# Performance work log

Measured on AMD Instinct MI355X. Metric: run time of the kernel, lower is better.

## Reference

```python
import jax, jax.numpy as jnp
import numpy as np
import math

B, T, P, E, H = 4, 64, 256, 512, 8
D = E // H
LN_EPS = 1e-5


def setup_inputs() -> dict:
    key = jax.random.key(0)
    ks = jax.random.split(key, 6)
    s = 0.02  # weight init scale
    return {
        "x": jax.random.normal(ks[0], (B, T, P, E), jnp.float32),
        "Wq": jax.random.normal(ks[1], (E, E), jnp.float32) * s,
        "bq": jnp.zeros((E,), jnp.float32),
        "Wk": jax.random.normal(ks[2], (E, E), jnp.float32) * s,
        "bk": jnp.zeros((E,), jnp.float32),
        "Wv": jax.random.normal(ks[3], (E, E), jnp.float32) * s,
        "bv": jnp.zeros((E,), jnp.float32),
        "Wo": jax.random.normal(ks[4], (E, E), jnp.float32) * s,
        "bo": jnp.zeros((E,), jnp.float32),
        "ln_g": jnp.ones((E,), jnp.float32),
        "ln_b": jnp.zeros((E,), jnp.float32),
    }


def _proj(x, W, b):
    # torch nn.Linear: y = x @ W.T + b
    return jnp.einsum('btpe,fe->btpf', x, W) + b


def _heads(y):
    # b t p (h d) -> b p h t d
    b, t, p, e = y.shape
    return y.reshape(b, t, p, H, D).transpose(0, 2, 3, 1, 4)


def reference(x, Wq, bq, Wk, bk, Wv, bv, Wo, bo, ln_g, ln_b):
    b, t, p, e = x.shape
    q = _heads(_proj(x, Wq, bq))  # [B,P,H,T,D]
    k = _heads(_proj(x, Wk, bk))
    v = _heads(_proj(x, Wv, bv))

    scores = jnp.einsum('bphtd,bphsd->bphts', q, k) / math.sqrt(D)
    causal_mask = jnp.triu(jnp.ones((t, t), dtype=bool), k=1)  # True above diag
    scores = jnp.where(causal_mask, -jnp.inf, scores)
    attn = jax.nn.softmax(scores, axis=-1)
    o = jnp.einsum('bphts,bphsd->bphtd', attn, v)

    # b p h t d -> b t p (h d)
    o = o.transpose(0, 3, 1, 2, 4).reshape(b, t, p, e)
    attn_out = jnp.einsum('btpe,fe->btpf', o, Wo) + bo

    y = x + attn_out
    # AdaptiveNormalizer with conditioning=None -> plain LayerNorm over E
    mu = jnp.mean(y, axis=-1, keepdims=True)
    var = jnp.var(y, axis=-1, keepdims=True)
    return (y - mu) * jax.lax.rsqrt(var + LN_EPS) * ln_g + ln_b
```

## Files before the change

### kernel.cpp

```cpp
#include <hip/hip_runtime.h>
#include <stdint.h>

#define B_ 4
#define T_ 64
#define P_ 256
#define E_ 512
#define H_ 8
#define D_ 64
#define NF 1536
#define MCH 16384

typedef unsigned short u16;
typedef __attribute__((ext_vector_type(8))) __bf16 bf16x8;
typedef __attribute__((ext_vector_type(4))) float f32x4;

__device__ __forceinline__ u16 f2bf(float x) {
  union { float f; uint32_t u; } a; a.f = x;
  uint32_t u = a.u;
  uint32_t r = (u + 0x7FFFu + ((u >> 16) & 1u)) >> 16;
  return (u16)r;
}

__device__ __forceinline__ bf16x8 ld8(const u16* p) {
  union { uint4 u; bf16x8 b; } t;
  t.u = *reinterpret_cast<const uint4*>(p);
  return t.b;
}

typedef __attribute__((address_space(3))) void lds_void;
typedef __attribute__((address_space(1))) void g_void;
__device__ __forceinline__ void gl_lds16(const void* g, void* l) {
  __builtin_amdgcn_global_load_lds((g_void*)g, (lds_void*)l, 16, 0, 0);
}

__device__ __forceinline__ f32x4 mfma16(bf16x8 a, bf16x8 b, f32x4 c) {
  return __builtin_amdgcn_mfma_f32_16x16x32_bf16(a, b, c, 0, 0, 0);
}

__global__ void cvt_bf16(const float* __restrict__ src, u16* __restrict__ dst, int n8) {
  int i = blockIdx.x * blockDim.x + threadIdx.x;
  if (i >= n8) return;
  const float4* s = reinterpret_cast<const float4*>(src) + (size_t)i * 2;
  float4 a = s[0], b = s[1];
  union { u16 u[8]; uint4 v; } t;
  t.u[0] = f2bf(a.x); t.u[1] = f2bf(a.y); t.u[2] = f2bf(a.z); t.u[3] = f2bf(a.w);
  t.u[4] = f2bf(b.x); t.u[5] = f2bf(b.y); t.u[6] = f2bf(b.z); t.u[7] = f2bf(b.w);
  reinterpret_cast<uint4*>(dst)[i] = t.v;
}

__global__ void cvt_w(const float* __restrict__ Wq, const float* __restrict__ Wk,
                      const float* __restrict__ Wv, const float* __restrict__ Wo,
                      u16* __restrict__ wqkv, u16* __restrict__ wobf) {
  int idx = blockIdx.x * blockDim.x + threadIdx.x;
  int w = idx >> 15;
  int off = idx & 32767;
  const float* s = (w == 0) ? Wq : (w == 1) ? Wk : (w == 2) ? Wv : Wo;
  const float4* sp = reinterpret_cast<const float4*>(s) + (size_t)off * 2;
  float4 a = sp[0], b = sp[1];
  union { u16 u[8]; uint4 v; } t;
  t.u[0] = f2bf(a.x); t.u[1] = f2bf(a.y); t.u[2] = f2bf(a.z); t.u[3] = f2bf(a.w);
  t.u[4] = f2bf(b.x); t.u[5] = f2bf(b.y); t.u[6] = f2bf(b.z); t.u[7] = f2bf(b.w);
  if (w < 3) reinterpret_cast<uint4*>(wqkv)[w * 32768 + off] = t.v;
  else       reinterpret_cast<uint4*>(wobf)[off] = t.v;
}

__global__ __launch_bounds__(256) void k1_qkv(
    const u16* __restrict__ xbf,
    const u16* __restrict__ wqkv,
    const float* __restrict__ bq, const float* __restrict__ bk, const float* __restrict__ bv,
    u16* __restrict__ qkv)
{
  __shared__ u16 As[2][128 * 64];
  __shared__ u16 Bs[2][128 * 64];
  const int tid = threadIdx.x;
  const int lane = tid & 63;
  const int wid = tid >> 6;
  const int m0 = blockIdx.y * 128;
  const int n0 = blockIdx.x * 128;
  const int wm = (wid >> 1) * 64;
  const int wn = (wid & 1) * 64;
  const int g4 = lane >> 4, l15 = lane & 15;
  const int lrow = lane >> 3;
  const int lcol = (lane & 7) * 8;

  f32x4 acc[4][4];
#pragma unroll
  for (int i = 0; i < 4; i++)
#pragma unroll
    for (int j = 0; j < 4; j++) { f32x4 z = {0.f, 0.f, 0.f, 0.f}; acc[i][j] = z; }

  const u16* ga = xbf + (size_t)m0 * E_;
  const u16* gb = wqkv + (size_t)n0 * E_;

  auto stage = [&](int buf, int kt) {
    const int k0 = kt * 64;
#pragma unroll
    for (int p = 0; p < 4; ++p) {
      const int ch = wid * 4 + p;
      const int r = ch * 8 + lrow;
      gl_lds16(ga + (size_t)r * E_ + k0 + lcol, &As[buf][ch * 512]);
      gl_lds16(gb + (size_t)r * E_ + k0 + lcol, &Bs[buf][ch * 512]);
    }
  };

  stage(0, 0);
  __syncthreads();
  int cur = 0;
  for (int kt = 0; kt < 8; ++kt) {
    if (kt < 7) stage(cur ^ 1, kt + 1);
#pragma unroll
    for (int ks = 0; ks < 2; ++ks) {
      const int fc = ks * 32 + g4 * 8;
      bf16x8 af[4], bfr[4];
#pragma unroll
      for (int mi = 0; mi < 4; mi++) af[mi] = ld8(&As[cur][(wm + mi * 16 + l15) * 64 + fc]);
#pragma unroll
      for (int ni = 0; ni < 4; ni++) bfr[ni] = ld8(&Bs[cur][(wn + ni * 16 + l15) * 64 + fc]);
#pragma unroll
      for (int mi = 0; mi < 4; mi++)
#pragma unroll
        for (int ni = 0; ni < 4; ni++)
          acc[mi][ni] = mfma16(af[mi], bfr[ni], acc[mi][ni]);
    }
    __syncthreads();
    cur ^= 1;
  }
#pragma unroll
  for (int ni = 0; ni < 4; ni++) {
    const int fcol = n0 + wn + ni * 16 + l15;
    const float bias = fcol < 512 ? bq[fcol] : (fcol < 1024 ? bk[fcol - 512] : bv[fcol - 1024]);
#pragma unroll
    for (int mi = 0; mi < 4; mi++)
#pragma unroll
      for (int r = 0; r < 4; r++) {
        const int row = m0 + wm + mi * 16 + g4 * 4 + r;
        qkv[(size_t)row * NF + fcol] = f2bf(acc[mi][ni][r] + bias);
      }
  }
}

__global__ __launch_bounds__(256) void k2_attn(
    const u16* __restrict__ qkv,
    u16* __restrict__ o)
{
  __shared__ u16 Pl[4][64 * 72];
  const int tid = threadIdx.x, lane = tid & 63, wid = tid >> 6;
  const int gw = blockIdx.x * 4 + wid;
  const int b = gw >> 11;
  const int g = gw & 2047;
  const int h = g & 7, p = g >> 3;
  const int g4 = lane >> 4;
  const size_t ts = (size_t)P_ * NF;
  const u16* qb = qkv + (size_t)b * MCH * NF + (size_t)p * NF + h * D_;
  const u16* kb = qb + 512;
  const u16* vb = qb + 1024;
  u16* ob = o + (size_t)b * MCH * E_;

  bf16x8 qf[4][2], kf[4][2];
#pragma unroll
  for (int i = 0; i < 4; i++)
#pragma unroll
    for (int ks = 0; ks < 2; ks++) {
      const int rr = i * 16 + (lane & 15);
      const int dc = ks * 32 + g4 * 8;
      qf[i][ks] = ld8(qb + (size_t)rr * ts + dc);
      kf[i][ks] = ld8(kb + (size_t)rr * ts + dc);
    }
  f32x4 S[4][4];
#pragma unroll
  for (int i = 0; i < 4; i++)
#pragma unroll
    for (int j = 0; j < 4; j++) { f32x4 z = {0.f, 0.f, 0.f, 0.f}; S[i][j] = z; }
#pragma unroll
  for (int ks = 0; ks < 2; ks++)
#pragma unroll
    for (int mi = 0; mi < 4; mi++)
#pragma unroll
      for (int ni = 0; ni < 4; ni++)
        S[mi][ni] = mfma16(qf[mi][ks], kf[ni][ks], S[mi][ni]);

  u16* pw = &Pl[wid][0];
#pragma unroll
  for (int mi = 0; mi < 4; mi++)
#pragma unroll
    for (int r = 0; r < 4; r++) {
      const int t = mi * 16 + g4 * 4 + r;
      float v[4]; float mx = -1e30f;
#pragma unroll
      for (int ni = 0; ni < 4; ni++) {
        const int s = ni * 16 + (lane & 15);
        v[ni] = (s <= t) ? S[mi][ni][r] * 0.125f : -1e30f;
        mx = fmaxf(mx, v[ni]);
      }
      mx = fmaxf(mx, __shfl_xor(mx, 1));
      mx = fmaxf(mx, __shfl_xor(mx, 2));
      mx = fmaxf(mx, __shfl_xor(mx, 4));
      mx = fmaxf(mx, __shfl_xor(mx, 8));
      float sum = 0.f; float pv[4];
#pragma unroll
      for (int ni = 0; ni < 4; ni++) {
        const int s = ni * 16 + (lane & 15);
        pv[ni] = (s <= t) ? __expf(v[ni] - mx) : 0.f;
        sum += pv[ni];
      }
      sum += __shfl_xor(sum, 1);
      sum += __shfl_xor(sum, 2);
      sum += __shfl_xor(sum, 4);
      sum += __shfl_xor(sum, 8);
      const float inv = 1.0f / sum;
#pragma unroll
      for (int ni = 0; ni < 4; ni++) {
        const int s = ni * 16 + (lane & 15);
        pw[t * 72 + s] = f2bf(pv[ni] * inv);
      }
    }
  __syncthreads();

  f32x4 O[4][4];
#pragma unroll
  for (int i = 0; i < 4; i++)
#pragma unroll
    for (int j = 0; j < 4; j++) { f32x4 z = {0.f, 0.f, 0.f, 0.f}; O[i][j] = z; }
#pragma unroll
  for (int ks = 0; ks < 2; ks++) {
    bf16x8 pa[4], vf[4];
#pragma unroll
    for (int mi = 0; mi < 4; mi++)
      pa[mi] = ld8(pw + (mi * 16 + (lane & 15)) * 72 + ks * 32 + g4 * 8);
#pragma unroll
    for (int ni = 0; ni < 4; ni++) {
      union { u16 u[8]; bf16x8 b; } tv;
#pragma unroll
      for (int j = 0; j < 8; j++) {
        const int s = ks * 32 + g4 * 8 + j;
        tv.u[j] = vb[(size_t)s * ts + ni * 16 + (lane & 15)];
      }
      vf[ni] = tv.b;
    }
#pragma unroll
    for (int mi = 0; mi < 4; mi++)
#pragma unroll
      for (int ni = 0; ni < 4; ni++)
        O[mi][ni] = mfma16(pa[mi], vf[ni], O[mi][ni]);
  }
#pragma unroll
  for (int mi = 0; mi < 4; mi++)
#pragma unroll
    for (int ni = 0; ni < 4; ni++)
#pragma unroll
      for (int r = 0; r < 4; r++) {
        const int t = mi * 16 + g4 * 4 + r;
        const int d = ni * 16 + (lane & 15);
        ob[((size_t)t * P_ + p) * E_ + h * D_ + d] = f2bf(O[mi][ni][r]);
      }
}

__global__ __launch_bounds__(512) void k3_out(
    const u16* __restrict__ obf,
    const u16* __restrict__ wo,
    const float* __restrict__ bo,
    const float* __restrict__ x,
    const float* __restrict__ lng, const float* __restrict__ lnb,
    float* __restrict__ out)
{
  __shared__ u16 As[2][128 * 32];
  __shared__ u16 Bs[2][512 * 32];
  __shared__ float redS[128][8];
  __shared__ float redQ[128][8];
  const int tid = threadIdx.x, lane = tid & 63, wid = tid >> 6;
  const int m0 = blockIdx.x * 128;
  const int g4 = lane >> 4, l15 = lane & 15;
  const int lr = lane >> 2;
  const int lc = (lane & 3) * 8;

  f32x4 acc[8][4];
#pragma unroll
  for (int i = 0; i < 8; i++)
#pragma unroll
    for (int j = 0; j < 4; j++) { f32x4 z = {0.f, 0.f, 0.f, 0.f}; acc[i][j] = z; }

  const u16* ga = obf + (size_t)m0 * E_;

  auto stage = [&](int buf, int kt) {
    const int k0 = kt * 32;
    gl_lds16(ga + (size_t)(wid * 16 + lr) * E_ + k0 + lc, &As[buf][wid * 512]);
#pragma unroll
    for (int p = 0; p < 4; ++p) {
      const int ch = wid * 4 + p;
      gl_lds16(wo + (size_t)(ch * 16 + lr) * E_ + k0 + lc, &Bs[buf][ch * 512]);
    }
  };

  stage(0, 0);
  __syncthreads();
  int cur = 0;
  for (int kt = 0; kt < 16; ++kt) {
    if (kt < 15) stage(cur ^ 1, kt + 1);
    const int fc = g4 * 8;
    bf16x8 af[8], bfr[4];
#pragma unroll
    for (int mi = 0; mi < 8; mi++) af[mi] = ld8(&As[cur][(mi * 16 + l15) * 32 + fc]);
#pragma unroll
    for (int ni = 0; ni < 4; ni++) bfr[ni] = ld8(&Bs[cur][(wid * 64 + ni * 16 + l15) * 32 + fc]);
#pragma unroll
    for (int mi = 0; mi < 8; mi++)
#pragma unroll
      for (int ni = 0; ni < 4; ni++)
        acc[mi][ni] = mfma16(af[mi], bfr[ni], acc[mi][ni]);
    __syncthreads();
    cur ^= 1;
  }

  float gg[4], bb[4], bof[4];
#pragma unroll
  for (int ni = 0; ni < 4; ni++) {
    const int f = wid * 64 + ni * 16 + l15;
    gg[ni] = lng[f]; bb[ni] = lnb[f]; bof[ni] = bo[f];
  }
#pragma unroll
  for (int mi = 0; mi < 8; mi++)
#pragma unroll
    for (int r = 0; r < 4; r++) {
      const int n = m0 + mi * 16 + g4 * 4 + r;
#pragma unroll
      for (int ni = 0; ni < 4; ni++) {
        const int f = wid * 64 + ni * 16 + l15;
        acc[mi][ni][r] += bof[ni] + x[(size_t)n * E_ + f];
      }
    }
#pragma unroll
  for (int mi = 0; mi < 8; mi++)
#pragma unroll
    for (int r = 0; r < 4; r++) {
      float s = 0.f, q = 0.f;
#pragma unroll
      for (int ni = 0; ni < 4; ni++) { const float y = acc[mi][ni][r]; s += y; q += y * y; }
      s += __shfl_xor(s, 1); q += __shfl_xor(q, 1);
      s += __shfl_xor(s, 2); q += __shfl_xor(q, 2);
      s += __shfl_xor(s, 4); q += __shfl_xor(q, 4);
      s += __shfl_xor(s, 8); q += __shfl_xor(q, 8);
      if (l15 == 0) {
        const int rl = mi * 16 + g4 * 4 + r;
        redS[rl][wid] = s; redQ[rl][wid] = q;
      }
    }
  __syncthreads();
#pragma unroll
  for (int mi = 0; mi < 8; mi++)
#pragma unroll
    for (int r = 0; r < 4; r++) {
      const int rl = mi * 16 + g4 * 4 + r;
      float Sx = 0.f, Qx = 0.f;
#pragma unroll
      for (int w = 0; w < 8; w++) { Sx += redS[rl][w]; Qx += redQ[rl][w]; }
      const float mean = Sx * (1.0f / 512.0f);
      const float var = Qx * (1.0f / 512.0f) - mean * mean;
      const float rs = rsqrtf(var + 1e-5f);
      const int n = m0 + rl;
#pragma unroll
      for (int ni = 0; ni < 4; ni++) {
        const int f = wid * 64 + ni * 16 + l15;
        out[(size_t)n * E_ + f] = (acc[mi][ni][r] - mean) * rs * gg[ni] + bb[ni];
      }
    }
}

extern "C" void kernel_launch(void* const* d_in, const int* in_sizes, int n_in,
                              void* d_out, int out_size, void* d_ws, size_t ws_size,
                              hipStream_t stream) {
  const float* x   = (const float*)d_in[0];
  const float* Wq  = (const float*)d_in[1];
  const float* bq  = (const float*)d_in[2];
  const float* Wk  = (const float*)d_in[3];
  const float* bk  = (const float*)d_in[4];
  const float* Wv  = (const float*)d_in[5];
  const float* bv  = (const float*)d_in[6];
  const float* Wo  = (const float*)d_in[7];
  const float* bo  = (const float*)d_in[8];
  const float* lng = (const float*)d_in[9];
  const float* lnb = (const float*)d_in[10];
  float* out = (float*)d_out;
  uint8_t* ws = (uint8_t*)d_ws;

  const size_t NEED_BIG = 270532608ULL;
  if (ws_size >= NEED_BIG) {
    u16* wqkv = (u16*)(ws);
    u16* wobf = (u16*)(ws + 1572864);
    u16* xbf  = (u16*)(ws + 2097152);
    u16* qkvc = (u16*)(ws + 69206016);
    u16* obf  = xbf;

    cvt_w<<<512, 256, 0, stream>>>(Wq, Wk, Wv, Wo, wqkv, wobf);
    cvt_bf16<<<16384, 256, 0, stream>>>(x, xbf, B_ * MCH * E_ / 8);
    k1_qkv<<<dim3(12, 512), 256, 0, stream>>>(xbf, wqkv, bq, bk, bv, qkvc);
    k2_attn<<<2048, 256, 0, stream>>>(qkvc, obf);
    k3_out<<<512, 512, 0, stream>>>(obf, wobf, bo, x, lng, lnb, out);
  } else {
    u16* xbf  = (u16*)(ws);
    u16* qkvc = (u16*)(ws + 16777216);
    u16* obf  = (u16*)(ws + 67108864);
    u16* wqkv = (u16*)(ws + 83886080);
    u16* wobf = (u16*)(ws + 85458944);

    cvt_w<<<512, 256, 0, stream>>>(Wq, Wk, Wv, Wo, wqkv, wobf);
    for (int b = 0; b < B_; ++b) {
      const float* xb = x + (size_t)b * MCH * E_;
      cvt_bf16<<<4096, 256, 0, stream>>>(xb, xbf, MCH * E_ / 8);
      k1_qkv<<<dim3(12, 128), 256, 0, stream>>>(xbf, wqkv, bq, bk, bv, qkvc);
      k2_attn<<<512, 256, 0, stream>>>(qkvc, obf);
      k3_out<<<128, 512, 0, stream>>>(obf, wobf, bo, xb, lng, lnb, out + (size_t)b * MCH * E_);
    }
  }
}
```

Baseline: 433.4 us.

## Rewrite QKV GEMM as 256x256 tile with 8 waves and fine-grained pipelining

The QKV projection kernel moves from 128x128 tiles with 4 waves to 256x256 tiles with 8 waves per block. It adds a half-K-step staged LDS pipeline with explicit vmcnt waits and barriers interleaved between MFMA groups, s_setprio around the MFMA bursts, and an XCD-aware block index remap. The aim is more data reuse per loaded tile and better overlap of global-to-LDS loads with matrix math. In exchange it uses 128KB of LDS and more accumulator registers, with a launch bound of 2 blocks per CU that may be hard to meet, and the hand-tuned wait counts are fragile.

Measured after the change: 440.0 us. No clear change (+1.5%).

```diff
diff --git a/kernel.cpp b/kernel.cpp
--- a/kernel.cpp
+++ b/kernel.cpp
@@ -36,6 +36,8 @@
 __device__ __forceinline__ f32x4 mfma16(bf16x8 a, bf16x8 b, f32x4 c) {
   return __builtin_amdgcn_mfma_f32_16x16x32_bf16(a, b, c, 0, 0, 0);
 }
+
+#define SBAR() __builtin_amdgcn_s_barrier()
 
 __global__ void cvt_bf16(const float* __restrict__ src, u16* __restrict__ dst, int n8) {
   int i = blockIdx.x * blockDim.x + threadIdx.x;
@@ -64,76 +66,115 @@
   else       reinterpret_cast<uint4*>(wobf)[off] = t.v;
 }
 
-__global__ __launch_bounds__(256) void k1_qkv(
+#define K1_MFMA(MB)                                                         \
+  __builtin_amdgcn_s_setprio(1);                                            \
+  _Pragma("unroll") for (int i = 0; i < 4; i++)                             \
+  _Pragma("unroll") for (int j = 0; j < 4; j++)                             \
+    acc[(MB) + i][j] = mfma16(af[i], bfv[j], acc[(MB) + i][j]);             \
+  __builtin_amdgcn_s_setprio(0);
+
+#define K1_READA(E, HH, MB)                                                 \
+  _Pragma("unroll") for (int i = 0; i < 4; i++)                             \
+    af[i] = ld8(ldsA + ((E) * 2 + (HH)) * 8192 +                            \
+                (wr * 128 + ((MB) + i) * 16 + l15) * 32 + g4 * 8);
+
+#define K1_READB(E, HH)                                                     \
+  _Pragma("unroll") for (int j = 0; j < 4; j++)                             \
+    bfv[j] = ld8(ldsB + ((E) * 2 + (HH)) * 8192 +                           \
+                 (wc * 64 + j * 16 + l15) * 32 + g4 * 8);
+
+__global__ __launch_bounds__(512, 2) void k1_qkv(
     const u16* __restrict__ xbf,
     const u16* __restrict__ wqkv,
     const float* __restrict__ bq, const float* __restrict__ bk, const float* __restrict__ bv,
     u16* __restrict__ qkv)
 {
-  __shared__ u16 As[2][128 * 64];
-  __shared__ u16 Bs[2][128 * 64];
+  __shared__ u16 lds[65536];
+  u16* ldsA = lds;
+  u16* ldsB = lds + 32768;
+
   const int tid = threadIdx.x;
-  const int lane = tid & 63;
-  const int wid = tid >> 6;
-  const int m0 = blockIdx.y * 128;
-  const int n0 = blockIdx.x * 128;
-  const int wm = (wid >> 1) * 64;
-  const int wn = (wid & 1) * 64;
+  const int lane = tid & 63, wid = tid >> 6;
+  const int wr = wid >> 2, wc = wid & 3;
   const int g4 = lane >> 4, l15 = lane & 15;
-  const int lrow = lane >> 3;
-  const int lcol = (lane & 7) * 8;
-
-  f32x4 acc[4][4];
-#pragma unroll
-  for (int i = 0; i < 4; i++)
-#pragma unroll
-    for (int j = 0; j < 4; j++) { f32x4 z = {0.f, 0.f, 0.f, 0.f}; acc[i][j] = z; }
+
+  const int cpx = gridDim.x >> 3;
+  const int logical = (blockIdx.x & 7) * cpx + (blockIdx.x >> 3);
+  const int m0 = (logical / 6) * 256;
+  const int n0 = (logical % 6) * 256;
 
   const u16* ga = xbf + (size_t)m0 * E_;
   const u16* gb = wqkv + (size_t)n0 * E_;
 
-  auto stage = [&](int buf, int kt) {
-    const int k0 = kt * 64;
-#pragma unroll
-    for (int p = 0; p < 4; ++p) {
-      const int ch = wid * 4 + p;
-      const int r = ch * 8 + lrow;
-      gl_lds16(ga + (size_t)r * E_ + k0 + lcol, &As[buf][ch * 512]);
-      gl_lds16(gb + (size_t)r * E_ + k0 + lcol, &Bs[buf][ch * 512]);
-    }
+  const int r0 = tid >> 2;
+  const int c0 = (tid & 3) * 8;
+
+  auto stageA = [&](int e, int h, int kt) {
+    const int kc = kt * 64 + h * 32;
+    u16* base = ldsA + (e * 2 + h) * 8192;
+    gl_lds16(ga + (size_t)r0 * E_ + kc + c0, base + wid * 512);
+    gl_lds16(ga + (size_t)(r0 + 128) * E_ + kc + c0, base + 4096 + wid * 512);
   };
-
-  stage(0, 0);
-  __syncthreads();
-  int cur = 0;
-  for (int kt = 0; kt < 8; ++kt) {
-    if (kt < 7) stage(cur ^ 1, kt + 1);
-#pragma unroll
-    for (int ks = 0; ks < 2; ++ks) {
-      const int fc = ks * 32 + g4 * 8;
-      bf16x8 af[4], bfr[4];
-#pragma unroll
-      for (int mi = 0; mi < 4; mi++) af[mi] = ld8(&As[cur][(wm + mi * 16 + l15) * 64 + fc]);
-#pragma unroll
-      for (int ni = 0; ni < 4; ni++) bfr[ni] = ld8(&Bs[cur][(wn + ni * 16 + l15) * 64 + fc]);
-#pragma unroll
-      for (int mi = 0; mi < 4; mi++)
-#pragma unroll
-        for (int ni = 0; ni < 4; ni++)
-          acc[mi][ni] = mfma16(af[mi], bfr[ni], acc[mi][ni]);
-    }
-    __syncthreads();
-    cur ^= 1;
-  }
+  auto stageB = [&](int e, int h, int kt) {
+    const int kc = kt * 64 + h * 32;
+    u16* base = ldsB + (e * 2 + h) * 8192;
+    gl_lds16(gb + (size_t)r0 * E_ + kc + c0, base + wid * 512);
+    gl_lds16(gb + (size_t)(r0 + 128) * E_ + kc + c0, base + 4096 + wid * 512);
+  };
+
+  f32x4 acc[8][4];
+#pragma unroll
+  for (int i = 0; i < 8; i++)
+#pragma unroll
+    for (int j = 0; j < 4; j++) { f32x4 z = {0.f, 0.f, 0.f, 0.f}; acc[i][j] = z; }
+
+  stageA(0, 0, 0); stageB(0, 0, 0);
+  stageA(0, 1, 0); stageB(0, 1, 0);
+  stageA(1, 0, 1); stageB(1, 0, 1);
+  asm volatile("s_waitcnt vmcnt(8)" ::: "memory");
+  SBAR();
+
+#pragma unroll 2
+  for (int s = 0; s < 8; ++s) {
+    const int e = s & 1;
+    bf16x8 af[4], bfv[4];
+    K1_READA(e, 0, 0)
+    K1_READB(e, 0)
+    if (s < 7) stageA(e ^ 1, 1, s + 1);
+    SBAR();
+    K1_MFMA(0)
+    SBAR();
+    K1_READA(e, 0, 4)
+    if (s < 7) stageB(e ^ 1, 1, s + 1);
+    if (s < 7) { asm volatile("s_waitcnt vmcnt(8)" ::: "memory"); }
+    else       { asm volatile("s_waitcnt vmcnt(0)" ::: "memory"); }
+    SBAR();
+    K1_MFMA(4)
+    SBAR();
+    K1_READA(e, 1, 0)
+    K1_READB(e, 1)
+    if (s < 6) stageA(e, 0, s + 2);
+    SBAR();
+    K1_MFMA(0)
+    SBAR();
+    K1_READA(e, 1, 4)
+    if (s < 6) stageB(e, 0, s + 2);
+    if (s < 6)      { asm volatile("s_waitcnt vmcnt(8)" ::: "memory"); }
+    else if (s == 6){ asm volatile("s_waitcnt vmcnt(4)" ::: "memory"); }
+    SBAR();
+    K1_MFMA(4)
+    SBAR();
+  }
+
 #pragma unroll
   for (int ni = 0; ni < 4; ni++) {
-    const int fcol = n0 + wn + ni * 16 + l15;
+    const int fcol = n0 + wc * 64 + ni * 16 + l15;
     const float bias = fcol < 512 ? bq[fcol] : (fcol < 1024 ? bk[fcol - 512] : bv[fcol - 1024]);
 #pragma unroll
-    for (int mi = 0; mi < 4; mi++)
+    for (int mi = 0; mi < 8; mi++)
 #pragma unroll
       for (int r = 0; r < 4; r++) {
-        const int row = m0 + wm + mi * 16 + g4 * 4 + r;
+        const int row = m0 + wr * 128 + mi * 16 + g4 * 4 + r;
         qkv[(size_t)row * NF + fcol] = f2bf(acc[mi][ni][r] + bias);
       }
   }
@@ -392,7 +433,7 @@
 
     cvt_w<<<512, 256, 0, stream>>>(Wq, Wk, Wv, Wo, wqkv, wobf);
     cvt_bf16<<<16384, 256, 0, stream>>>(x, xbf, B_ * MCH * E_ / 8);
-    k1_qkv<<<dim3(12, 512), 256, 0, stream>>>(xbf, wqkv, bq, bk, bv, qkvc);
+    k1_qkv<<<1536, 512, 0, stream>>>(xbf, wqkv, bq, bk, bv, qkvc);
     k2_attn<<<2048, 256, 0, stream>>>(qkvc, obf);
     k3_out<<<512, 512, 0, stream>>>(obf, wobf, bo, x, lng, lnb, out);
   } else {
@@ -406,7 +447,7 @@
     for (int b = 0; b < B_; ++b) {
       const float* xb = x + (size_t)b * MCH * E_;
       cvt_bf16<<<4096, 256, 0, stream>>>(xb, xbf, MCH * E_ / 8);
-      k1_qkv<<<dim3(12, 128), 256, 0, stream>>>(xbf, wqkv, bq, bk, bv, qkvc);
+      k1_qkv<<<384, 512, 0, stream>>>(xbf, wqkv, bq, bk, bv, qkvc);
       k2_attn<<<512, 256, 0, stream>>>(qkvc, obf);
       k3_out<<<128, 512, 0, stream>>>(obf, wobf, bo, xb, lng, lnb, out + (size_t)b * MCH * E_);
     }
```
